# Performance work log

Hardware: AMD Instinct MI355X
Metric: run time of the kernel (lower is better)

## Reference

```python
import jax, jax.numpy as jnp
import numpy as np

DIM = 768
N_HEADS = 12
HEAD_DIM = DIM // N_HEADS
B, S = 2, 4096


def setup_inputs() -> dict:
    key = jax.random.key(0)
    k_x, k_wqkv, k_bqkv, k_wout, k_bout = jax.random.split(key, 5)
    scale_in = 1.0 / np.sqrt(DIM)
    return {
        "x": jax.random.normal(k_x, (B, S, DIM), dtype=jnp.float32),
        "Wqkv": jax.random.normal(k_wqkv, (DIM, 3 * DIM), dtype=jnp.float32) * scale_in,
        "bqkv": jax.random.normal(k_bqkv, (3 * DIM,), dtype=jnp.float32) * 0.02,
        "Wout": jax.random.normal(k_wout, (DIM, DIM), dtype=jnp.float32) * scale_in,
        "bout": jax.random.normal(k_bout, (DIM,), dtype=jnp.float32) * 0.02,
    }


def reference(x, Wqkv, bqkv, Wout, bout):
    b, s, d = x.shape
    qkv = (x @ Wqkv + bqkv).reshape(b, s, 3, N_HEADS, HEAD_DIM)
    qkv = jnp.transpose(qkv, (2, 0, 3, 1, 4))  # [3, B, H, S, hd]
    q, k, v = qkv[0], qkv[1], qkv[2]
    scale = HEAD_DIM ** -0.5
    attn = jnp.einsum('bhqd,bhkd->bhqk', q, k) * scale  # [B, H, S, S]
    causal_mask = jnp.triu(jnp.ones((s, s), dtype=bool), k=1)
    attn = jnp.where(causal_mask[None, None], -jnp.inf, attn)
    attn = jax.nn.softmax(attn, axis=-1)
    out = jnp.einsum('bhqk,bhkd->bhqd', attn, v)  # [B, H, S, hd]
    out = jnp.transpose(out, (0, 2, 1, 3)).reshape(b, s, d)
    return out @ Wout + bout
```

## Files before the change

### kernel.cpp

```cpp
#include <hip/hip_runtime.h>
#include <hip/hip_bf16.h>
#include <math.h>

#define DIM 768
#define NH 12
#define HD 64
#define BATCH 2
#define SEQ 4096
#define MTOT (BATCH * SEQ)

#define QSCALE 0.1803368801111244f

typedef unsigned short u16;
typedef __bf16 bf16x8 __attribute__((ext_vector_type(8)));
typedef float  f32x4  __attribute__((ext_vector_type(4)));
typedef float  f32x16 __attribute__((ext_vector_type(16)));
typedef unsigned short u16x4 __attribute__((ext_vector_type(4)));
typedef unsigned short u16x8 __attribute__((ext_vector_type(8)));
typedef unsigned u32x4 __attribute__((ext_vector_type(4)));

__device__ inline u16 f2bf(float f) {
    unsigned u = __builtin_bit_cast(unsigned, f);
    u += 0x7fffu + ((u >> 16) & 1u);
    return (u16)(u >> 16);
}

#if defined(__has_builtin) && __has_builtin(__builtin_amdgcn_cvt_pk_bf16_f32)
#define HAVE_PK_BF16 1
__device__ inline unsigned pk2bf(float a, float b) {
    auto v = __builtin_amdgcn_cvt_pk_bf16_f32(a, b);
    return __builtin_bit_cast(unsigned, v);
}
#else
#define HAVE_PK_BF16 0
__device__ inline unsigned pk2bf(float a, float b) {
    return (unsigned)f2bf(a) | ((unsigned)f2bf(b) << 16);
}
#endif

__device__ inline f32x16 mfma32(bf16x8 a, bf16x8 b, f32x16 c) {
    return __builtin_amdgcn_mfma_f32_32x32x16_bf16(a, b, c, 0, 0, 0);
}

__device__ inline void gl2lds16(const u16* g, u16* l) {
    __builtin_amdgcn_global_load_lds(
        (const __attribute__((address_space(1))) void*)g,
        (__attribute__((address_space(3))) void*)l,
        16, 0, 0);
}

__global__ __launch_bounds__(256)
void cvt_bf16(const float* __restrict__ src, u16* __restrict__ dst, int n8)
{
    int i = blockIdx.x * 256 + threadIdx.x;
    if (i >= n8) return;
    float4 a = ((const float4*)src)[i * 2];
    float4 b = ((const float4*)src)[i * 2 + 1];
    u16x8 o;
    o[0] = f2bf(a.x); o[1] = f2bf(a.y); o[2] = f2bf(a.z); o[3] = f2bf(a.w);
    o[4] = f2bf(b.x); o[5] = f2bf(b.y); o[6] = f2bf(b.z); o[7] = f2bf(b.w);
    ((u16x8*)dst)[i] = o;
}

__global__ __launch_bounds__(256)
void transpose_to_bf16(const float* __restrict__ src, u16* __restrict__ dst,
                       int R, int C)
{
    __shared__ float tile[32][33];
    const int c0 = blockIdx.x * 32, r0 = blockIdx.y * 32;
    const int tx = threadIdx.x & 31, ty = threadIdx.x >> 5;
#pragma unroll
    for (int i = 0; i < 4; ++i) {
        int row = ty * 4 + i;
        tile[row][tx] = src[(size_t)(r0 + row) * C + c0 + tx];
    }
    __syncthreads();
#pragma unroll
    for (int i = 0; i < 4; ++i) {
        int crow = ty * 4 + i;
        dst[(size_t)(c0 + crow) * R + r0 + tx] = f2bf(tile[tx][crow]);
    }
}

__device__ inline void gemm_lds_mainloop(const u16* __restrict__ Ag,
                                         const u16* __restrict__ Bg,
                                         int m0, int n0, int w, int lane,
                                         u16 (*As)[64 * 64], u16 (*Bs)[64 * 64],
                                         f32x16 acc[2][2])
{
    const int lc32 = lane & 31, hi = lane >> 5;
    const int wm = (w & 1) * 64, wn = (w >> 1) * 64;
    const int drow = lane >> 3;
    const int dp   = lane & 7;

#pragma unroll
    for (int mi = 0; mi < 2; ++mi)
#pragma unroll
        for (int nj = 0; nj < 2; ++nj)
            acc[mi][nj] = f32x16{};

    int trA[2], kcA[2], lr0[2];
#pragma unroll
    for (int i = 0; i < 2; ++i) {
        const int r = w * 16 + i * 8 + drow;
        const int g = dp ^ (r & 7);
        trA[i] = 2 * r + (g >> 2);
        kcA[i] = g & 3;
        lr0[i] = (w * 16 + i * 8) * 64;
    }

#pragma unroll
    for (int i = 0; i < 2; ++i) {
        gl2lds16(Ag + (size_t)(m0 + trA[i]) * 768 + kcA[i] * 8, &As[0][lr0[i]]);
        gl2lds16(Bg + (size_t)(n0 + trA[i]) * 768 + kcA[i] * 8, &Bs[0][lr0[i]]);
    }
#pragma unroll
    for (int i = 0; i < 2; ++i) {
        gl2lds16(Ag + (size_t)(m0 + trA[i]) * 768 + 32 + kcA[i] * 8, &As[1][lr0[i]]);
        gl2lds16(Bg + (size_t)(n0 + trA[i]) * 768 + 32 + kcA[i] * 8, &Bs[1][lr0[i]]);
    }

    int cur = 0;
    for (int ks = 0; ks < 24; ++ks) {
        if (ks + 1 < 24) { asm volatile("s_waitcnt vmcnt(4)" ::: "memory"); }
        else             { asm volatile("s_waitcnt vmcnt(0)" ::: "memory"); }
        __builtin_amdgcn_s_barrier();

        if (ks + 2 < 24) {
            const int nb = (cur >= 1) ? (cur - 1) : 2;
            const int k0 = (ks + 2) * 32;
#pragma unroll
            for (int i = 0; i < 2; ++i) {
                gl2lds16(Ag + (size_t)(m0 + trA[i]) * 768 + k0 + kcA[i] * 8,
                         &As[nb][lr0[i]]);
                gl2lds16(Bg + (size_t)(n0 + trA[i]) * 768 + k0 + kcA[i] * 8,
                         &Bs[nb][lr0[i]]);
            }
        }

        bf16x8 af[2][2], bfr[2][2];
#pragma unroll
        for (int mi = 0; mi < 2; ++mi)
#pragma unroll
            for (int kh = 0; kh < 2; ++kh) {
                const int m = wm + mi * 32 + lc32;
                const int r = m >> 1;
                const int p = ((m & 1) * 4 + kh * 2 + hi) ^ (r & 7);
                af[mi][kh] = *(const bf16x8*)&As[cur][r * 64 + p * 8];
            }
#pragma unroll
        for (int nj = 0; nj < 2; ++nj)
#pragma unroll
            for (int kh = 0; kh < 2; ++kh) {
                const int n = wn + nj * 32 + lc32;
                const int r = n >> 1;
                const int p = ((n & 1) * 4 + kh * 2 + hi) ^ (r & 7);
                bfr[nj][kh] = *(const bf16x8*)&Bs[cur][r * 64 + p * 8];
            }

        __builtin_amdgcn_s_setprio(1);
#pragma unroll
        for (int mi = 0; mi < 2; ++mi)
#pragma unroll
            for (int nj = 0; nj < 2; ++nj) {
                acc[mi][nj] = mfma32(af[mi][0], bfr[nj][0], acc[mi][nj]);
                acc[mi][nj] = mfma32(af[mi][1], bfr[nj][1], acc[mi][nj]);
            }
        __builtin_amdgcn_s_setprio(0);

        cur = (cur == 2) ? 0 : cur + 1;
    }
}

__global__ __launch_bounds__(256, 3)
void gemm_qkv_mfma(const u16* __restrict__ A, const u16* __restrict__ Bt,
                   const float* __restrict__ bias,
                   u16* __restrict__ Qb, u16* __restrict__ Kb, u16* __restrict__ Vt)
{
    __shared__ u16 As[3][64 * 64];
    __shared__ u16 Bs[3][64 * 64];
    const int m0 = blockIdx.x * 128;
    const int n0 = blockIdx.y * 128;
    const int t = threadIdx.x;
    const int w = t >> 6, lane = t & 63;
    const int lc32 = lane & 31, hi = lane >> 5;
    const int wm = (w & 1) * 64, wn = (w >> 1) * 64;

    f32x16 acc[2][2];
    gemm_lds_mainloop(A, Bt, m0, n0, w, lane, As, Bs, acc);

    const int b  = m0 >> 12;
    const int s0 = (m0 & 4095) + wm;
    const int nbase = n0 + wn;
    const int three = nbase / 768;
    const int rem   = nbase - three * 768;
    const int h     = rem >> 6;
    const int bh    = b * NH + h;

    if (three < 2) {
        u16* dst = (three == 0) ? Qb : Kb;
        const float qs = (three == 0) ? QSCALE : 1.0f;
#pragma unroll
        for (int nj = 0; nj < 2; ++nj) {
            const int d = nj * 32 + lc32;
            const float bi = bias[nbase + d];
#pragma unroll
            for (int mi = 0; mi < 2; ++mi)
#pragma unroll
                for (int r = 0; r < 16; ++r) {
                    const int s = s0 + mi * 32 + (r & 3) + 8 * (r >> 2) + 4 * hi;
                    dst[((size_t)bh * SEQ + s) * HD + d] = f2bf((acc[mi][nj][r] + bi) * qs);
                }
        }
    } else {
#pragma unroll
        for (int nj = 0; nj < 2; ++nj) {
            const int d = nj * 32 + lc32;
            const float bi = bias[nbase + d];
            const size_t rowb = ((size_t)bh * HD + d) * SEQ;
#pragma unroll
            for (int mi = 0; mi < 2; ++mi)
#pragma unroll
                for (int g = 0; g < 4; ++g) {
                    const int s = s0 + mi * 32 + 8 * g + 4 * hi;
                    u16x4 wv;
#pragma unroll
                    for (int rr = 0; rr < 4; ++rr)
                        wv[rr] = f2bf(acc[mi][nj][g * 4 + rr] + bi);
                    *(u16x4*)&Vt[rowb + s] = wv;
                }
        }
    }
}

__global__ __launch_bounds__(256, 3)
void gemm_out_mfma(const u16* __restrict__ A, const u16* __restrict__ Bt,
                   const float* __restrict__ bias, float* __restrict__ C)
{
    __shared__ u16 As[3][64 * 64];
    __shared__ u16 Bs[3][64 * 64];
    const int m0 = blockIdx.x * 128;
    const int n0 = blockIdx.y * 128;
    const int t = threadIdx.x;
    const int w = t >> 6, lane = t & 63;
    const int lc32 = lane & 31, hi = lane >> 5;
    const int wm = (w & 1) * 64, wn = (w >> 1) * 64;

    f32x16 acc[2][2];
    gemm_lds_mainloop(A, Bt, m0, n0, w, lane, As, Bs, acc);

#pragma unroll
    for (int nj = 0; nj < 2; ++nj) {
        const int col = n0 + wn + nj * 32 + lc32;
        const float bi = bias[col];
#pragma unroll
        for (int mi = 0; mi < 2; ++mi)
#pragma unroll
            for (int r = 0; r < 16; ++r) {
                const int row = m0 + wm + mi * 32 + (r & 3) + 8 * (r >> 2) + 4 * hi;
                C[(size_t)row * 768 + col] = acc[mi][nj][r] + bi;
            }
    }
}

__global__ __launch_bounds__(256, 4)
void flash_attn(const u16* __restrict__ Qg, const u16* __restrict__ Kg,
                const u16* __restrict__ Vtg, u16* __restrict__ Og)
{
    const int bh   = blockIdx.x;
    const int qt   = 63 - (int)blockIdx.y;
    const int b    = bh / NH, h = bh % NH;
    const int t    = threadIdx.x;
    const int w    = t >> 6;
    const int wq   = w >> 1;
    const int wk   = w & 1;
    const int lane = t & 63;
    const int lc32 = lane & 31;
    const int hi   = lane >> 5;
    const int drow = lane >> 3;
    const int dp   = lane & 7;

    __shared__ u16 Ks[2][64 * 64];
    __shared__ u16 Vs[2][64 * 64];

    const u16* Qp = Qg  + (size_t)bh * SEQ * HD;
    const u16* Kp = Kg  + (size_t)bh * SEQ * HD;
    const u16* Vp = Vtg + (size_t)bh * HD * SEQ;
    float* Vscr = (float*)&Vs[0][0];
    float* Lx   = (float*)&Ks[0][0];

    const int qrow0 = qt * 64 + wq * 32;

    bf16x8 qa[4];
#pragma unroll
    for (int ds = 0; ds < 4; ++ds)
        qa[ds] = *(const bf16x8*)
            &Qp[(size_t)(qrow0 + lc32) * HD + ds * 16 + hi * 8];

    f32x16 o2[2];
    o2[0] = f32x16{};
    o2[1] = f32x16{};
    float l_r = 0.f;

#pragma unroll
    for (int i = 0; i < 2; ++i) {
        const int r0  = w * 16 + i * 8;
        const int row = r0 + drow;
        const int gc  = dp ^ (row & 7);
        gl2lds16(Kp + (size_t)row * HD + gc * 8, &Ks[0][r0 * 64]);
        gl2lds16(Vp + (size_t)row * SEQ + gc * 8, &Vs[0][r0 * 64]);
    }
    __syncthreads();

    for (int tk = 0; tk <= qt; ++tk) {
        const int kb  = tk * 64;
        const int cur = tk & 1;

        if (tk < qt) {
            const int kbn = kb + 64;
#pragma unroll
            for (int i = 0; i < 2; ++i) {
                const int r0  = w * 16 + i * 8;
                const int row = r0 + drow;
                const int gc  = dp ^ (row & 7);
                gl2lds16(Kp + (size_t)(kbn + row) * HD + gc * 8,
                         &Ks[1 - cur][r0 * 64]);
                gl2lds16(Vp + (size_t)row * SEQ + kbn + gc * 8,
                         &Vs[1 - cur][r0 * 64]);
            }
        }

        f32x16 sacc = {};
        {
            const int row = wk * 32 + lc32;
            const int sw  = row & 7;
            __builtin_amdgcn_s_setprio(1);
#pragma unroll
            for (int ds = 0; ds < 4; ++ds) {
                bf16x8 kf = *(const bf16x8*)
                    &Ks[cur][row * 64 + (((ds * 2 + hi) ^ sw) * 8)];
                sacc = mfma32(kf, qa[ds], sacc);
            }
            __builtin_amdgcn_s_setprio(0);
        }

        if (tk == qt) {
            const int q = qrow0 + lc32;
#pragma unroll
            for (int r = 0; r < 16; ++r) {
                const int key = kb + wk * 32 + (r & 3) + 8 * (r >> 2) + 4 * hi;
                if (key > q) sacc[r] = -1e30f;
            }
        }

        float pv[16];
#pragma unroll
        for (int r = 0; r < 16; ++r)
            pv[r] = __builtin_amdgcn_exp2f(sacc[r]);

        l_r += (((pv[0] + pv[1]) + (pv[2] + pv[3]))
              + ((pv[4] + pv[5]) + (pv[6] + pv[7])))
             + (((pv[8] + pv[9]) + (pv[10] + pv[11]))
              + ((pv[12] + pv[13]) + (pv[14] + pv[15])));

        bf16x8 pa[2];
#pragma unroll
        for (int s = 0; s < 2; ++s) {
            unsigned w0 = pk2bf(pv[8 * s + 0], pv[8 * s + 1]);
            unsigned w1 = pk2bf(pv[8 * s + 2], pv[8 * s + 3]);
            unsigned w2 = pk2bf(pv[8 * s + 4], pv[8 * s + 5]);
            unsigned w3 = pk2bf(pv[8 * s + 6], pv[8 * s + 7]);
            asm("v_permlane32_swap_b32 %0, %1" : "+v"(w0), "+v"(w2));
            asm("v_permlane32_swap_b32 %0, %1" : "+v"(w1), "+v"(w3));
            u32x4 tw;
            tw[0] = w0; tw[1] = w1; tw[2] = w2; tw[3] = w3;
            pa[s] = __builtin_bit_cast(bf16x8, tw);
        }

        __builtin_amdgcn_s_setprio(1);
#pragma unroll
        for (int dt = 0; dt < 2; ++dt) {
            const int row = dt * 32 + lc32;
            const int sw  = row & 7;
#pragma unroll
            for (int s = 0; s < 2; ++s) {
                bf16x8 vf = *(const bf16x8*)
                    &Vs[cur][row * 64 + (((wk * 4 + s * 2 + hi) ^ sw) * 8)];
                o2[dt] = mfma32(pa[s], vf, o2[dt]);
            }
        }
        __builtin_amdgcn_s_setprio(0);

        __syncthreads();
    }

    const float lt = l_r + __shfl_xor(l_r, 32);

    if (wk == 1) {
#pragma unroll
        for (int dt = 0; dt < 2; ++dt)
#pragma unroll
            for (int r = 0; r < 16; ++r) {
                const int ql = (r & 3) + 8 * (r >> 2) + 4 * hi;
                Vscr[wq * 2048 + ql * 64 + dt * 32 + lc32] = o2[dt][r];
            }
        if (lane < 32) Lx[wq * 32 + lc32] = lt;
    }
    __syncthreads();
    if (wk == 0) {
        const float linv_q = 1.0f / (lt + Lx[wq * 32 + lc32]);
#pragma unroll
        for (int r = 0; r < 16; ++r) {
            const int ql   = (r & 3) + 8 * (r >> 2) + 4 * hi;
            const float li = __shfl(linv_q, ql);
            const int q = qrow0 + ql;
            const size_t base = ((size_t)(b * SEQ + q)) * DIM + h * HD + lc32;
#pragma unroll
            for (int dt = 0; dt < 2; ++dt) {
                const float ov = o2[dt][r]
                    + Vscr[wq * 2048 + ql * 64 + dt * 32 + lc32];
                Og[base + dt * 32] = f2bf(ov * li);
            }
        }
    }
}

extern "C" void kernel_launch(void* const* d_in, const int* in_sizes, int n_in,
                              void* d_out, int out_size, void* d_ws, size_t ws_size,
                              hipStream_t stream)
{
    const float* x    = (const float*)d_in[0];
    const float* Wqkv = (const float*)d_in[1];
    const float* bqkv = (const float*)d_in[2];
    const float* Wout = (const float*)d_in[3];
    const float* bout = (const float*)d_in[4];
    float* out = (float*)d_out;

    const size_t NX  = (size_t)MTOT * DIM;
    const size_t NWQ = (size_t)DIM * 3 * DIM;
    const size_t NWO = (size_t)DIM * DIM;
    u16* p   = (u16*)d_ws;
    u16* Xb  = p;              p += NX;
    u16* Wqt = p;              p += NWQ;
    u16* Wot = p;              p += NWO;
    u16* Qb  = p;              p += NX;
    u16* Kb  = p;              p += NX;
    u16* Vt  = p;              p += NX;
    u16* Ao  = p;

    cvt_bf16<<<(int)(NX / 8 + 255) / 256, 256, 0, stream>>>(x, Xb, (int)(NX / 8));
    transpose_to_bf16<<<dim3(2304 / 32, 768 / 32), 256, 0, stream>>>(Wqkv, Wqt, 768, 2304);
    transpose_to_bf16<<<dim3(768 / 32, 768 / 32), 256, 0, stream>>>(Wout, Wot, 768, 768);

    gemm_qkv_mfma<<<dim3(MTOT / 128, 2304 / 128), 256, 0, stream>>>(Xb, Wqt, bqkv, Qb, Kb, Vt);
    flash_attn<<<dim3(24, 64), 256, 0, stream>>>(Qb, Kb, Vt, Ao);
    gemm_out_mfma<<<dim3(MTOT / 128, 768 / 128), 256, 0, stream>>>(Ao, Wot, bout, out);
}
```

Baseline: 235.6 us.

## Fuse prep kernels into one launch and stage V-transpose stores through LDS

Merges the x conversion and the two weight transpose kernels into a single launch that dispatches on block index, removing two kernel launches. In the QKV GEMM epilogue, the V tile is first written to LDS scratch (padded rows), then read back and written to the transposed Vt with coalesced 8-byte stores along the sequence. Each lane previously issued scattered 8-byte stores across rows. The LDS staging adds a barrier and extra shared-memory traffic in the epilogue.

```diff
diff --git a/kernel.cpp b/kernel.cpp
--- a/kernel.cpp
+++ b/kernel.cpp
@@ -50,24 +50,33 @@
 }
 
 __global__ __launch_bounds__(256)
-void cvt_bf16(const float* __restrict__ src, u16* __restrict__ dst, int n8)
-{
-    int i = blockIdx.x * 256 + threadIdx.x;
-    if (i >= n8) return;
-    float4 a = ((const float4*)src)[i * 2];
-    float4 b = ((const float4*)src)[i * 2 + 1];
-    u16x8 o;
-    o[0] = f2bf(a.x); o[1] = f2bf(a.y); o[2] = f2bf(a.z); o[3] = f2bf(a.w);
-    o[4] = f2bf(b.x); o[5] = f2bf(b.y); o[6] = f2bf(b.z); o[7] = f2bf(b.w);
-    ((u16x8*)dst)[i] = o;
-}
-
-__global__ __launch_bounds__(256)
-void transpose_to_bf16(const float* __restrict__ src, u16* __restrict__ dst,
-                       int R, int C)
-{
+void prep_fused(const float* __restrict__ x, u16* __restrict__ Xb,
+                const float* __restrict__ Wqkv, u16* __restrict__ Wqt,
+                const float* __restrict__ Wout, u16* __restrict__ Wot)
+{
+    const int bid = blockIdx.x;
+    if (bid < 3072) {
+        const int i = bid * 256 + threadIdx.x;
+        float4 a = ((const float4*)x)[i * 2];
+        float4 b = ((const float4*)x)[i * 2 + 1];
+        u16x8 o;
+        o[0] = f2bf(a.x); o[1] = f2bf(a.y); o[2] = f2bf(a.z); o[3] = f2bf(a.w);
+        o[4] = f2bf(b.x); o[5] = f2bf(b.y); o[6] = f2bf(b.z); o[7] = f2bf(b.w);
+        ((u16x8*)Xb)[i] = o;
+        return;
+    }
     __shared__ float tile[32][33];
-    const int c0 = blockIdx.x * 32, r0 = blockIdx.y * 32;
+    const float* src; u16* dst; int R, C, bx, by;
+    if (bid < 3072 + 1728) {
+        const int t2 = bid - 3072;
+        src = Wqkv; dst = Wqt; R = 768; C = 2304;
+        bx = t2 % 72; by = t2 / 72;
+    } else {
+        const int t2 = bid - 4800;
+        src = Wout; dst = Wot; R = 768; C = 768;
+        bx = t2 % 24; by = t2 / 24;
+    }
+    const int c0 = bx * 32, r0 = by * 32;
     const int tx = threadIdx.x & 31, ty = threadIdx.x >> 5;
 #pragma unroll
     for (int i = 0; i < 4; ++i) {
@@ -189,6 +198,8 @@
     f32x16 acc[2][2];
     gemm_lds_mainloop(A, Bt, m0, n0, w, lane, As, Bs, acc);
 
+    __syncthreads();
+
     const int b  = m0 >> 12;
     const int s0 = (m0 & 4095) + wm;
     const int nbase = n0 + wn;
@@ -213,22 +224,27 @@
                 }
         }
     } else {
+        u16* scr = (w < 2) ? (&As[0][0] + w * 4352)
+                           : (&Bs[0][0] + (w - 2) * 4352);
 #pragma unroll
         for (int nj = 0; nj < 2; ++nj) {
             const int d = nj * 32 + lc32;
             const float bi = bias[nbase + d];
-            const size_t rowb = ((size_t)bh * HD + d) * SEQ;
 #pragma unroll
             for (int mi = 0; mi < 2; ++mi)
 #pragma unroll
-                for (int g = 0; g < 4; ++g) {
-                    const int s = s0 + mi * 32 + 8 * g + 4 * hi;
-                    u16x4 wv;
-#pragma unroll
-                    for (int rr = 0; rr < 4; ++rr)
-                        wv[rr] = f2bf(acc[mi][nj][g * 4 + rr] + bi);
-                    *(u16x4*)&Vt[rowb + s] = wv;
+                for (int r = 0; r < 16; ++r) {
+                    const int s = mi * 32 + (r & 3) + 8 * (r >> 2) + 4 * hi;
+                    scr[d * 68 + s] = f2bf(acc[mi][nj][r] + bi);
                 }
+        }
+        const size_t vbase = (size_t)bh * HD * SEQ + s0;
+#pragma unroll
+        for (int p = 0; p < 16; ++p) {
+            const int d = p * 4 + (lane >> 4);
+            const int s = (lane & 15) * 4;
+            u16x4 v4 = *(const u16x4*)&scr[d * 68 + s];
+            *(u16x4*)&Vt[vbase + (size_t)d * SEQ + s] = v4;
         }
     }
 }
@@ -448,9 +464,7 @@
     u16* Vt  = p;              p += NX;
     u16* Ao  = p;
 
-    cvt_bf16<<<(int)(NX / 8 + 255) / 256, 256, 0, stream>>>(x, Xb, (int)(NX / 8));
-    transpose_to_bf16<<<dim3(2304 / 32, 768 / 32), 256, 0, stream>>>(Wqkv, Wqt, 768, 2304);
-    transpose_to_bf16<<<dim3(768 / 32, 768 / 32), 256, 0, stream>>>(Wout, Wot, 768, 768);
+    prep_fused<<<3072 + 1728 + 576, 256, 0, stream>>>(x, Xb, Wqkv, Wqt, Wout, Wot);
 
     gemm_qkv_mfma<<<dim3(MTOT / 128, 2304 / 128), 256, 0, stream>>>(Xb, Wqt, bqkv, Qb, Kb, Vt);
     flash_attn<<<dim3(24, 64), 256, 0, stream>>>(Qb, Kb, Vt, Ao);
```

Result: faster. 230.2 us, median of 2 (-2.3%).
